# Optimization experiments

Hardware: AMD Instinct MI355X
Metric: run time of the kernel (lower is better)

Reference implementation:

```python
import jax, jax.numpy as jnp
import numpy as np
from jax import lax
from functools import partial

NPOINT = 2048
RADIUS = 1.0
NSAMPLE = 32


def _fps(xyz, npoint):
    # Farthest point sampling, sequential as in the classic CUDA kernel.
    # xyz: (N, 3) -> (npoint,) int32 indices; starts at index 0.
    N = xyz.shape[0]
    init_d = jnp.full((N,), jnp.inf, dtype=xyz.dtype)

    def step(carry, _):
        dists, last = carry
        delta = xyz - xyz[last]                      # (N, 3)
        nd = jnp.sum(delta * delta, axis=-1)         # (N,)
        dists = jnp.minimum(dists, nd)
        nxt = jnp.argmax(dists).astype(jnp.int32)
        return (dists, nxt), last

    (_, _), idxs = lax.scan(step, (init_d, jnp.int32(0)), None, length=npoint)
    return idxs


def _ball_query(radius, nsample, xyz, new_xyz):
    # xyz: (N, 3), new_xyz: (S, 3) -> (S, nsample) int32.
    # Take the first nsample points (in original order) within radius of each
    # centroid; pad with the first found index (centroid itself always hits).
    N = xyz.shape[0]
    d2 = (jnp.sum(new_xyz * new_xyz, -1, keepdims=True)
          + jnp.sum(xyz * xyz, -1)[None, :]
          - 2.0 * new_xyz @ xyz.T)                   # (S, N)
    mask = d2 < radius * radius
    key = jnp.where(mask, jnp.arange(N, dtype=jnp.int32), jnp.int32(N))  # (S, N)
    neg_topk, _ = lax.top_k(-key, nsample)           # nsample smallest keys
    idx = -neg_topk                                  # (S, nsample), ascending
    first = idx[:, :1]
    return jnp.where(idx == N, first, idx)


def setup_inputs() -> dict:
    key = jax.random.key(0)
    inputs = jax.random.normal(key, (4, 8192, 16), dtype=jnp.float32)
    return {"inputs": inputs}


def reference(inputs):
    xyz = inputs[..., :3]                            # (B, N, 3)
    points = inputs[..., 3:]                         # (B, N, C)

    fps_idx = jax.vmap(lambda p: _fps(p, NPOINT))(xyz)          # (B, S)
    new_xyz = jnp.take_along_axis(xyz, fps_idx[..., None], axis=1)  # (B, S, 3)

    idx = jax.vmap(partial(_ball_query, RADIUS, NSAMPLE))(xyz, new_xyz)  # (B, S, K)

    gather = jax.vmap(lambda p, i: p[i])             # (N, C), (S, K) -> (S, K, C)
    grouped_xyz = gather(xyz, idx) - new_xyz[:, :, None, :]      # (B, S, K, 3)
    grouped_points = gather(points, idx)                         # (B, S, K, C)
    new_points = jnp.concatenate([grouped_xyz, grouped_points], axis=-1)
    return new_xyz, new_points, idx, grouped_xyz
```

## Files before the change

### kernel.cpp

```cpp
#include <hip/hip_runtime.h>

#pragma clang fp contract(off)

#define NPOINT 2048
#define NSAMPLE 32
#define NPTS 8192
#define NB 4
#define CH 16
#define FPS_THREADS 512
#define PTS_PER_THREAD (NPTS / FPS_THREADS)
#define PAIRS (PTS_PER_THREAD / 2)
#define FPS_WAVES (FPS_THREADS / 64)

typedef unsigned long long u64;
typedef float v2f __attribute__((ext_vector_type(2)));

#define OFF_NEWXYZ 0
#define OFF_NEWPTS (NB * NPOINT * 3)
#define OFF_IDX (OFF_NEWPTS + NB * NPOINT * NSAMPLE * CH)
#define OFF_GXYZ (OFF_IDX + NB * NPOINT * NSAMPLE)

template <int CTRL>
__device__ __forceinline__ float dpp_fmax(float v) {
  int o = __builtin_amdgcn_update_dpp(0, __float_as_int(v), CTRL, 0xf, 0xf, true);
  return fmaxf(v, __int_as_float(o));
}

__global__ __launch_bounds__(FPS_THREADS)
__attribute__((amdgpu_waves_per_eu(2))) void fps_kernel(
    const float* __restrict__ in, float* __restrict__ out) {
  __shared__ float4 lpxyz[NPTS];
  __shared__ float newb[NPOINT * 3];
  __shared__ alignas(16) u64 slots[2][FPS_WAVES];

  const int b = blockIdx.x;
  const int tid = threadIdx.x;
  const int lane = tid & 63;
  const int wv = tid >> 6;
  const float* base = in + (size_t)b * NPTS * CH;

  v2f pxv[PAIRS], pyv[PAIRS], pzv[PAIRS], dv[PAIRS];
#pragma unroll
  for (int jp = 0; jp < PAIRS; ++jp) {
    int p0 = tid * PTS_PER_THREAD + 2 * jp;
    float4 r0 = *reinterpret_cast<const float4*>(base + (size_t)p0 * CH);
    float4 r1 = *reinterpret_cast<const float4*>(base + (size_t)(p0 + 1) * CH);
    pxv[jp] = (v2f){r0.x, r1.x};
    pyv[jp] = (v2f){r0.y, r1.y};
    pzv[jp] = (v2f){r0.z, r1.z};
    lpxyz[p0] = r0;
    lpxyz[p0 + 1] = r1;
    dv[jp] = (v2f){__builtin_inff(), __builtin_inff()};
  }
  if (tid < FPS_WAVES)
    slots[0][tid] = (tid == 0) ? (((u64)0x7f800000u << 32) | 8191u) : 0ull;

  for (int it = 0; it < NPOINT; ++it) {
    __syncthreads();
    const ulonglong2* sp =
        reinterpret_cast<const ulonglong2*>(&slots[it & 1][0]);
    const ulonglong2 s01 = sp[0];
    const ulonglong2 s23 = sp[1];
    const ulonglong2 s45 = sp[2];
    const ulonglong2 s67 = sp[3];
    u64 ka = (s01.y > s01.x) ? s01.y : s01.x;
    u64 kb = (s23.y > s23.x) ? s23.y : s23.x;
    u64 kc = (s45.y > s45.x) ? s45.y : s45.x;
    u64 kd = (s67.y > s67.x) ? s67.y : s67.x;
    ka = (kb > ka) ? kb : ka;
    kc = (kd > kc) ? kd : kc;
    const u64 k = (kc > ka) ? kc : ka;
    const int gi = 8191 - (int)(unsigned)k;
    const float4 g = lpxyz[gi];
    const float gx = g.x, gy = g.y, gz = g.z;
    if (tid == 0) {
      newb[it * 3 + 0] = gx;
      newb[it * 3 + 1] = gy;
      newb[it * 3 + 2] = gz;
    }
    float bestv = -1.0f;
    float bestx = -1.0f;
    int bestjp = 0;
#pragma unroll
    for (int jp = 0; jp < PAIRS; ++jp) {
      v2f dx = pxv[jp] - gx;
      v2f dy = pyv[jp] - gy;
      v2f dz = pzv[jp] - gz;
      v2f nd = (dx * dx + dy * dy) + dz * dz;
      v2f dn = {fminf(dv[jp].x, nd.x), fminf(dv[jp].y, nd.y)};
      dv[jp] = dn;
      float pm = fmaxf(dn.x, dn.y);
      bool t = pm > bestv;
      bestjp = t ? jp : bestjp;
      bestx = t ? dn.x : bestx;
      bestv = fmaxf(bestv, pm);
    }
    const int bestj = 2 * bestjp + ((bestx == bestv) ? 0 : 1);
    const unsigned besti = (unsigned)(tid * PTS_PER_THREAD + bestj);
    float wm = bestv;
    wm = dpp_fmax<0x111>(wm);
    wm = dpp_fmax<0x112>(wm);
    wm = dpp_fmax<0x114>(wm);
    wm = dpp_fmax<0x118>(wm);
    wm = dpp_fmax<0x142>(wm);
    wm = dpp_fmax<0x143>(wm);
    const float swm =
        __int_as_float(__builtin_amdgcn_readlane(__float_as_int(wm), 63));
    const u64 wbal = __ballot(bestv == swm);
    const int wl = (int)__builtin_ctzll(wbal);
    if (lane == wl) {
      slots[(it + 1) & 1][wv] =
          ((u64)__float_as_uint(bestv) << 32) | (8191u - besti);
    }
  }
  __syncthreads();
  float* ob = out + OFF_NEWXYZ + (size_t)b * NPOINT * 3;
  for (int i = tid; i < NPOINT * 3; i += FPS_THREADS) ob[i] = newb[i];
}

__device__ __forceinline__ void write_slot(float* __restrict__ out,
                                           const float* __restrict__ base,
                                           int b, int qi, int s, int p,
                                           float4 r0, float qx, float qy,
                                           float qz) {
  float dx = __fsub_rn(r0.x, qx);
  float dy = __fsub_rn(r0.y, qy);
  float dz = __fsub_rn(r0.z, qz);
  size_t qs = (size_t)b * NPOINT + qi;
  out[OFF_IDX + qs * NSAMPLE + s] = (float)p;
  float* g = out + OFF_GXYZ + (qs * NSAMPLE + s) * 3;
  g[0] = dx;
  g[1] = dy;
  g[2] = dz;
  const float* row = base + (size_t)p * CH;
  float4 r1 = *reinterpret_cast<const float4*>(row + 4);
  float4 r2 = *reinterpret_cast<const float4*>(row + 8);
  float4 r3 = *reinterpret_cast<const float4*>(row + 12);
  float* np_ = out + OFF_NEWPTS + (qs * NSAMPLE + s) * CH;
  *reinterpret_cast<float4*>(np_ + 0) = make_float4(dx, dy, dz, r0.w);
  *reinterpret_cast<float4*>(np_ + 4) = r1;
  *reinterpret_cast<float4*>(np_ + 8) = r2;
  *reinterpret_cast<float4*>(np_ + 12) = r3;
}

__global__ __launch_bounds__(256) void ballq_kernel(
    const float* __restrict__ in, float* __restrict__ out) {
  const int lane = threadIdx.x & 63;
  const int qid = blockIdx.x * 4 + (threadIdx.x >> 6);
  const int b = qid >> 11;
  const int qi = qid & 2047;
  const float* base = in + (size_t)b * NPTS * CH;
  const float* q = out + OFF_NEWXYZ + ((size_t)b * NPOINT + qi) * 3;
  float qx = q[0], qy = q[1], qz = q[2];
  float qn = __fadd_rn(__fadd_rn(__fmul_rn(qx, qx), __fmul_rn(qy, qy)),
                       __fmul_rn(qz, qz));

  int cnt = 0;
  int first = 0;
  bool have_first = false;
  for (int cg = 0; cg < NPTS / 64 && cnt < NSAMPLE; cg += 4) {
    float4 r[4];
#pragma unroll
    for (int u = 0; u < 4; ++u)
      r[u] = *reinterpret_cast<const float4*>(
          base + (size_t)((cg + u) * 64 + lane) * CH);
#pragma unroll
    for (int u = 0; u < 4; ++u) {
      const int chunk = cg + u;
      const int p = chunk * 64 + lane;
      const float4 r0 = r[u];
      float pn =
          __fadd_rn(__fadd_rn(__fmul_rn(r0.x, r0.x), __fmul_rn(r0.y, r0.y)),
                    __fmul_rn(r0.z, r0.z));
      float dot =
          __fadd_rn(__fadd_rn(__fmul_rn(qx, r0.x), __fmul_rn(qy, r0.y)),
                    __fmul_rn(qz, r0.z));
      float d2 = __fsub_rn(__fadd_rn(qn, pn), __fmul_rn(2.0f, dot));
      bool in_r = d2 < 1.0f;
      unsigned long long mask = __ballot(in_r);
      if (!have_first && mask) {
        first = chunk * 64 + __builtin_ctzll(mask);
        have_first = true;
      }
      int pos = cnt + __popcll(mask & ((1ull << lane) - 1ull));
      if (in_r && pos < NSAMPLE)
        write_slot(out, base, b, qi, pos, p, r0, qx, qy, qz);
      cnt += __popcll(mask);
    }
  }
  if (cnt < NSAMPLE) {
    int s = cnt + lane;
    if (s < NSAMPLE) {
      float4 r0 = *reinterpret_cast<const float4*>(base + (size_t)first * CH);
      write_slot(out, base, b, qi, s, first, r0, qx, qy, qz);
    }
  }
}

extern "C" void kernel_launch(void* const* d_in, const int* in_sizes, int n_in,
                              void* d_out, int out_size, void* d_ws,
                              size_t ws_size, hipStream_t stream) {
  (void)in_sizes;
  (void)n_in;
  (void)out_size;
  (void)d_ws;
  (void)ws_size;
  const float* in = (const float*)d_in[0];
  float* out = (float*)d_out;
  fps_kernel<<<NB, FPS_THREADS, 0, stream>>>(in, out);
  ballq_kernel<<<(NB * NPOINT) / 4, 256, 0, stream>>>(in, out);
}
```

Measured before the change: 1.840 ms.

## Fuse FPS and ball query into one persistent kernel with progress flags

```diff
diff --git a/kernel.cpp b/kernel.cpp
--- a/kernel.cpp
+++ b/kernel.cpp
@@ -11,6 +11,8 @@
 #define PTS_PER_THREAD (NPTS / FPS_THREADS)
 #define PAIRS (PTS_PER_THREAD / 2)
 #define FPS_WAVES (FPS_THREADS / 64)
+#define BQ_BLOCKS 252
+#define BQ_WAVES (BQ_BLOCKS * 8)
 
 typedef unsigned long long u64;
 typedef float v2f __attribute__((ext_vector_type(2)));
@@ -24,98 +26,6 @@
 __device__ __forceinline__ float dpp_fmax(float v) {
   int o = __builtin_amdgcn_update_dpp(0, __float_as_int(v), CTRL, 0xf, 0xf, true);
   return fmaxf(v, __int_as_float(o));
-}
-
-__global__ __launch_bounds__(FPS_THREADS)
-__attribute__((amdgpu_waves_per_eu(2))) void fps_kernel(
-    const float* __restrict__ in, float* __restrict__ out) {
-  __shared__ float4 lpxyz[NPTS];
-  __shared__ float newb[NPOINT * 3];
-  __shared__ alignas(16) u64 slots[2][FPS_WAVES];
-
-  const int b = blockIdx.x;
-  const int tid = threadIdx.x;
-  const int lane = tid & 63;
-  const int wv = tid >> 6;
-  const float* base = in + (size_t)b * NPTS * CH;
-
-  v2f pxv[PAIRS], pyv[PAIRS], pzv[PAIRS], dv[PAIRS];
-#pragma unroll
-  for (int jp = 0; jp < PAIRS; ++jp) {
-    int p0 = tid * PTS_PER_THREAD + 2 * jp;
-    float4 r0 = *reinterpret_cast<const float4*>(base + (size_t)p0 * CH);
-    float4 r1 = *reinterpret_cast<const float4*>(base + (size_t)(p0 + 1) * CH);
-    pxv[jp] = (v2f){r0.x, r1.x};
-    pyv[jp] = (v2f){r0.y, r1.y};
-    pzv[jp] = (v2f){r0.z, r1.z};
-    lpxyz[p0] = r0;
-    lpxyz[p0 + 1] = r1;
-    dv[jp] = (v2f){__builtin_inff(), __builtin_inff()};
-  }
-  if (tid < FPS_WAVES)
-    slots[0][tid] = (tid == 0) ? (((u64)0x7f800000u << 32) | 8191u) : 0ull;
-
-  for (int it = 0; it < NPOINT; ++it) {
-    __syncthreads();
-    const ulonglong2* sp =
-        reinterpret_cast<const ulonglong2*>(&slots[it & 1][0]);
-    const ulonglong2 s01 = sp[0];
-    const ulonglong2 s23 = sp[1];
-    const ulonglong2 s45 = sp[2];
-    const ulonglong2 s67 = sp[3];
-    u64 ka = (s01.y > s01.x) ? s01.y : s01.x;
-    u64 kb = (s23.y > s23.x) ? s23.y : s23.x;
-    u64 kc = (s45.y > s45.x) ? s45.y : s45.x;
-    u64 kd = (s67.y > s67.x) ? s67.y : s67.x;
-    ka = (kb > ka) ? kb : ka;
-    kc = (kd > kc) ? kd : kc;
-    const u64 k = (kc > ka) ? kc : ka;
-    const int gi = 8191 - (int)(unsigned)k;
-    const float4 g = lpxyz[gi];
-    const float gx = g.x, gy = g.y, gz = g.z;
-    if (tid == 0) {
-      newb[it * 3 + 0] = gx;
-      newb[it * 3 + 1] = gy;
-      newb[it * 3 + 2] = gz;
-    }
-    float bestv = -1.0f;
-    float bestx = -1.0f;
-    int bestjp = 0;
-#pragma unroll
-    for (int jp = 0; jp < PAIRS; ++jp) {
-      v2f dx = pxv[jp] - gx;
-      v2f dy = pyv[jp] - gy;
-      v2f dz = pzv[jp] - gz;
-      v2f nd = (dx * dx + dy * dy) + dz * dz;
-      v2f dn = {fminf(dv[jp].x, nd.x), fminf(dv[jp].y, nd.y)};
-      dv[jp] = dn;
-      float pm = fmaxf(dn.x, dn.y);
-      bool t = pm > bestv;
-      bestjp = t ? jp : bestjp;
-      bestx = t ? dn.x : bestx;
-      bestv = fmaxf(bestv, pm);
-    }
-    const int bestj = 2 * bestjp + ((bestx == bestv) ? 0 : 1);
-    const unsigned besti = (unsigned)(tid * PTS_PER_THREAD + bestj);
-    float wm = bestv;
-    wm = dpp_fmax<0x111>(wm);
-    wm = dpp_fmax<0x112>(wm);
-    wm = dpp_fmax<0x114>(wm);
-    wm = dpp_fmax<0x118>(wm);
-    wm = dpp_fmax<0x142>(wm);
-    wm = dpp_fmax<0x143>(wm);
-    const float swm =
-        __int_as_float(__builtin_amdgcn_readlane(__float_as_int(wm), 63));
-    const u64 wbal = __ballot(bestv == swm);
-    const int wl = (int)__builtin_ctzll(wbal);
-    if (lane == wl) {
-      slots[(it + 1) & 1][wv] =
-          ((u64)__float_as_uint(bestv) << 32) | (8191u - besti);
-    }
-  }
-  __syncthreads();
-  float* ob = out + OFF_NEWXYZ + (size_t)b * NPOINT * 3;
-  for (int i = tid; i < NPOINT * 3; i += FPS_THREADS) ob[i] = newb[i];
 }
 
 __device__ __forceinline__ void write_slot(float* __restrict__ out,
@@ -143,18 +53,14 @@
   *reinterpret_cast<float4*>(np_ + 12) = r3;
 }
 
-__global__ __launch_bounds__(256) void ballq_kernel(
-    const float* __restrict__ in, float* __restrict__ out) {
-  const int lane = threadIdx.x & 63;
-  const int qid = blockIdx.x * 4 + (threadIdx.x >> 6);
-  const int b = qid >> 11;
-  const int qi = qid & 2047;
+__device__ __forceinline__ void ballq_one(const float* __restrict__ in,
+                                          float* __restrict__ out, int b,
+                                          int qi, int lane) {
   const float* base = in + (size_t)b * NPTS * CH;
   const float* q = out + OFF_NEWXYZ + ((size_t)b * NPOINT + qi) * 3;
   float qx = q[0], qy = q[1], qz = q[2];
   float qn = __fadd_rn(__fadd_rn(__fmul_rn(qx, qx), __fmul_rn(qy, qy)),
                        __fmul_rn(qz, qz));
-
   int cnt = 0;
   int first = 0;
   bool have_first = false;
@@ -197,16 +103,235 @@
   }
 }
 
+__global__ __launch_bounds__(FPS_THREADS)
+__attribute__((amdgpu_waves_per_eu(2))) void fused_kernel(
+    const float* __restrict__ in, float* __restrict__ out,
+    unsigned* __restrict__ prog) {
+  __shared__ float4 lpxyz[NPTS];
+  __shared__ float newb[NPOINT * 3];
+  __shared__ alignas(16) u64 slots[2][FPS_WAVES];
+
+  const int tid = threadIdx.x;
+  const int lane = tid & 63;
+
+  if (blockIdx.x >= NB) {
+    const int slot = (blockIdx.x - NB) * 8 + (tid >> 6);
+    for (int g = slot; g < NB * NPOINT; g += BQ_WAVES) {
+      const int qi = g >> 2;
+      const int b = g & 3;
+      for (;;) {
+        unsigned p = __hip_atomic_load(&prog[b], __ATOMIC_ACQUIRE,
+                                       __HIP_MEMORY_SCOPE_AGENT);
+        if (p > (unsigned)qi) break;
+        __builtin_amdgcn_s_sleep(32);
+      }
+      ballq_one(in, out, b, qi, lane);
+    }
+    return;
+  }
+
+  const int b = blockIdx.x;
+  const int wv = tid >> 6;
+  const float* base = in + (size_t)b * NPTS * CH;
+  float* gnew = out + OFF_NEWXYZ + (size_t)b * NPOINT * 3;
+
+  v2f pxv[PAIRS], pyv[PAIRS], pzv[PAIRS], dv[PAIRS];
+#pragma unroll
+  for (int jp = 0; jp < PAIRS; ++jp) {
+    int p0 = tid * PTS_PER_THREAD + 2 * jp;
+    float4 r0 = *reinterpret_cast<const float4*>(base + (size_t)p0 * CH);
+    float4 r1 = *reinterpret_cast<const float4*>(base + (size_t)(p0 + 1) * CH);
+    pxv[jp] = (v2f){r0.x, r1.x};
+    pyv[jp] = (v2f){r0.y, r1.y};
+    pzv[jp] = (v2f){r0.z, r1.z};
+    lpxyz[p0] = r0;
+    lpxyz[p0 + 1] = r1;
+    dv[jp] = (v2f){__builtin_inff(), __builtin_inff()};
+  }
+  if (tid < FPS_WAVES)
+    slots[0][tid] = (tid == 0) ? (((u64)0x7f800000u << 32) | 8191u) : 0ull;
+
+  for (int it = 0; it < NPOINT; ++it) {
+    __syncthreads();
+    const ulonglong2* sp =
+        reinterpret_cast<const ulonglong2*>(&slots[it & 1][0]);
+    const ulonglong2 s01 = sp[0];
+    const ulonglong2 s23 = sp[1];
+    const ulonglong2 s45 = sp[2];
+    const ulonglong2 s67 = sp[3];
+    u64 ka = (s01.y > s01.x) ? s01.y : s01.x;
+    u64 kb = (s23.y > s23.x) ? s23.y : s23.x;
+    u64 kc = (s45.y > s45.x) ? s45.y : s45.x;
+    u64 kd = (s67.y > s67.x) ? s67.y : s67.x;
+    ka = (kb > ka) ? kb : ka;
+    kc = (kd > kc) ? kd : kc;
+    const u64 k = (kc > ka) ? kc : ka;
+    const int gi = 8191 - (int)(unsigned)k;
+    const float4 g = lpxyz[gi];
+    const float gx = g.x, gy = g.y, gz = g.z;
+    if (tid == 0) {
+      newb[it * 3 + 0] = gx;
+      newb[it * 3 + 1] = gy;
+      newb[it * 3 + 2] = gz;
+    }
+    if ((it & 15) == 0 && it >= 16 && tid < 48)
+      gnew[(it - 16) * 3 + tid] = newb[(it - 16) * 3 + tid];
+    if ((it & 15) == 1 && it > 16 && tid == 0)
+      __hip_atomic_store(&prog[b], (unsigned)(it - 1), __ATOMIC_RELEASE,
+                         __HIP_MEMORY_SCOPE_AGENT);
+    float bestv = -1.0f;
+    float bestx = -1.0f;
+    int bestjp = 0;
+#pragma unroll
+    for (int jp = 0; jp < PAIRS; ++jp) {
+      v2f dx = pxv[jp] - gx;
+      v2f dy = pyv[jp] - gy;
+      v2f dz = pzv[jp] - gz;
+      v2f nd = (dx * dx + dy * dy) + dz * dz;
+      v2f dn = {fminf(dv[jp].x, nd.x), fminf(dv[jp].y, nd.y)};
+      dv[jp] = dn;
+      float pm = fmaxf(dn.x, dn.y);
+      bool t = pm > bestv;
+      bestjp = t ? jp : bestjp;
+      bestx = t ? dn.x : bestx;
+      bestv = fmaxf(bestv, pm);
+    }
+    const int bestj = 2 * bestjp + ((bestx == bestv) ? 0 : 1);
+    const unsigned besti = (unsigned)(tid * PTS_PER_THREAD + bestj);
+    float wm = bestv;
+    wm = dpp_fmax<0x111>(wm);
+    wm = dpp_fmax<0x112>(wm);
+    wm = dpp_fmax<0x114>(wm);
+    wm = dpp_fmax<0x118>(wm);
+    wm = dpp_fmax<0x142>(wm);
+    wm = dpp_fmax<0x143>(wm);
+    const float swm =
+        __int_as_float(__builtin_amdgcn_readlane(__float_as_int(wm), 63));
+    const u64 wbal = __ballot(bestv == swm);
+    const int wl = (int)__builtin_ctzll(wbal);
+    if (lane == wl) {
+      slots[(it + 1) & 1][wv] =
+          ((u64)__float_as_uint(bestv) << 32) | (8191u - besti);
+    }
+  }
+  __syncthreads();
+  if (tid < 48) gnew[2032 * 3 + tid] = newb[2032 * 3 + tid];
+  __syncthreads();
+  if (tid == 0)
+    __hip_atomic_store(&prog[b], (unsigned)NPOINT, __ATOMIC_RELEASE,
+                       __HIP_MEMORY_SCOPE_AGENT);
+}
+
+__global__ __launch_bounds__(FPS_THREADS)
+__attribute__((amdgpu_waves_per_eu(2))) void fps_kernel(
+    const float* __restrict__ in, float* __restrict__ out) {
+  __shared__ float4 lpxyz[NPTS];
+  __shared__ float newb[NPOINT * 3];
+  __shared__ alignas(16) u64 slots[2][FPS_WAVES];
+  const int b = blockIdx.x;
+  const int tid = threadIdx.x;
+  const int lane = tid & 63;
+  const int wv = tid >> 6;
+  const float* base = in + (size_t)b * NPTS * CH;
+  v2f pxv[PAIRS], pyv[PAIRS], pzv[PAIRS], dv[PAIRS];
+#pragma unroll
+  for (int jp = 0; jp < PAIRS; ++jp) {
+    int p0 = tid * PTS_PER_THREAD + 2 * jp;
+    float4 r0 = *reinterpret_cast<const float4*>(base + (size_t)p0 * CH);
+    float4 r1 = *reinterpret_cast<const float4*>(base + (size_t)(p0 + 1) * CH);
+    pxv[jp] = (v2f){r0.x, r1.x};
+    pyv[jp] = (v2f){r0.y, r1.y};
+    pzv[jp] = (v2f){r0.z, r1.z};
+    lpxyz[p0] = r0;
+    lpxyz[p0 + 1] = r1;
+    dv[jp] = (v2f){__builtin_inff(), __builtin_inff()};
+  }
+  if (tid < FPS_WAVES)
+    slots[0][tid] = (tid == 0) ? (((u64)0x7f800000u << 32) | 8191u) : 0ull;
+  for (int it = 0; it < NPOINT; ++it) {
+    __syncthreads();
+    const ulonglong2* sp =
+        reinterpret_cast<const ulonglong2*>(&slots[it & 1][0]);
+    const ulonglong2 s01 = sp[0];
+    const ulonglong2 s23 = sp[1];
+    const ulonglong2 s45 = sp[2];
+    const ulonglong2 s67 = sp[3];
+    u64 ka = (s01.y > s01.x) ? s01.y : s01.x;
+    u64 kb = (s23.y > s23.x) ? s23.y : s23.x;
+    u64 kc = (s45.y > s45.x) ? s45.y : s45.x;
+    u64 kd = (s67.y > s67.x) ? s67.y : s67.x;
+    ka = (kb > ka) ? kb : ka;
+    kc = (kd > kc) ? kd : kc;
+    const u64 k = (kc > ka) ? kc : ka;
+    const int gi = 8191 - (int)(unsigned)k;
+    const float4 g = lpxyz[gi];
+    const float gx = g.x, gy = g.y, gz = g.z;
+    if (tid == 0) {
+      newb[it * 3 + 0] = gx;
+      newb[it * 3 + 1] = gy;
+      newb[it * 3 + 2] = gz;
+    }
+    float bestv = -1.0f;
+    float bestx = -1.0f;
+    int bestjp = 0;
+#pragma unroll
+    for (int jp = 0; jp < PAIRS; ++jp) {
+      v2f dx = pxv[jp] - gx;
+      v2f dy = pyv[jp] - gy;
+      v2f dz = pzv[jp] - gz;
+      v2f nd = (dx * dx + dy * dy) + dz * dz;
+      v2f dn = {fminf(dv[jp].x, nd.x), fminf(dv[jp].y, nd.y)};
+      dv[jp] = dn;
+      float pm = fmaxf(dn.x, dn.y);
+      bool t = pm > bestv;
+      bestjp = t ? jp : bestjp;
+      bestx = t ? dn.x : bestx;
+      bestv = fmaxf(bestv, pm);
+    }
+    const int bestj = 2 * bestjp + ((bestx == bestv) ? 0 : 1);
+    const unsigned besti = (unsigned)(tid * PTS_PER_THREAD + bestj);
+    float wm = bestv;
+    wm = dpp_fmax<0x111>(wm);
+    wm = dpp_fmax<0x112>(wm);
+    wm = dpp_fmax<0x114>(wm);
+    wm = dpp_fmax<0x118>(wm);
+    wm = dpp_fmax<0x142>(wm);
+    wm = dpp_fmax<0x143>(wm);
+    const float swm =
+        __int_as_float(__builtin_amdgcn_readlane(__float_as_int(wm), 63));
+    const u64 wbal = __ballot(bestv == swm);
+    const int wl = (int)__builtin_ctzll(wbal);
+    if (lane == wl) {
+      slots[(it + 1) & 1][wv] =
+          ((u64)__float_as_uint(bestv) << 32) | (8191u - besti);
+    }
+  }
+  __syncthreads();
+  float* ob = out + OFF_NEWXYZ + (size_t)b * NPOINT * 3;
+  for (int i = tid; i < NPOINT * 3; i += FPS_THREADS) ob[i] = newb[i];
+}
+
+__global__ __launch_bounds__(256) void ballq_kernel(
+    const float* __restrict__ in, float* __restrict__ out) {
+  const int lane = threadIdx.x & 63;
+  const int qid = blockIdx.x * 4 + (threadIdx.x >> 6);
+  ballq_one(in, out, qid >> 11, qid & 2047, lane);
+}
+
 extern "C" void kernel_launch(void* const* d_in, const int* in_sizes, int n_in,
                               void* d_out, int out_size, void* d_ws,
                               size_t ws_size, hipStream_t stream) {
   (void)in_sizes;
   (void)n_in;
   (void)out_size;
-  (void)d_ws;
-  (void)ws_size;
   const float* in = (const float*)d_in[0];
   float* out = (float*)d_out;
-  fps_kernel<<<NB, FPS_THREADS, 0, stream>>>(in, out);
-  ballq_kernel<<<(NB * NPOINT) / 4, 256, 0, stream>>>(in, out);
-}
+  if (d_ws != nullptr && ws_size >= NB * sizeof(unsigned)) {
+    unsigned* prog = (unsigned*)d_ws;
+    hipMemsetAsync(prog, 0, NB * sizeof(unsigned), stream);
+    fused_kernel<<<NB + BQ_BLOCKS, FPS_THREADS, 0, stream>>>(in, out, prog);
+  } else {
+    fps_kernel<<<NB, FPS_THREADS, 0, stream>>>(in, out);
+    ballq_kernel<<<(NB * NPOINT) / 4, 256, 0, stream>>>(in, out);
+  }
+}
```

Result: slower. 2.124 ms (+15.4%).

## Fuse FPS and ball query into one persistent kernel with spin-wait streaming

Applied to the files above, without the earlier changes.

```diff
diff --git a/kernel.cpp b/kernel.cpp
--- a/kernel.cpp
+++ b/kernel.cpp
@@ -11,6 +11,9 @@
 #define PTS_PER_THREAD (NPTS / FPS_THREADS)
 #define PAIRS (PTS_PER_THREAD / 2)
 #define FPS_WAVES (FPS_THREADS / 64)
+#define BQ_BLOCKS 252
+#define BQ_WAVES (BQ_BLOCKS * 8)
+#define SENT 0xFFFFFFFFu
 
 typedef unsigned long long u64;
 typedef float v2f __attribute__((ext_vector_type(2)));
@@ -26,96 +29,16 @@
   return fmaxf(v, __int_as_float(o));
 }
 
-__global__ __launch_bounds__(FPS_THREADS)
-__attribute__((amdgpu_waves_per_eu(2))) void fps_kernel(
-    const float* __restrict__ in, float* __restrict__ out) {
-  __shared__ float4 lpxyz[NPTS];
-  __shared__ float newb[NPOINT * 3];
-  __shared__ alignas(16) u64 slots[2][FPS_WAVES];
-
-  const int b = blockIdx.x;
-  const int tid = threadIdx.x;
-  const int lane = tid & 63;
-  const int wv = tid >> 6;
-  const float* base = in + (size_t)b * NPTS * CH;
-
-  v2f pxv[PAIRS], pyv[PAIRS], pzv[PAIRS], dv[PAIRS];
-#pragma unroll
-  for (int jp = 0; jp < PAIRS; ++jp) {
-    int p0 = tid * PTS_PER_THREAD + 2 * jp;
-    float4 r0 = *reinterpret_cast<const float4*>(base + (size_t)p0 * CH);
-    float4 r1 = *reinterpret_cast<const float4*>(base + (size_t)(p0 + 1) * CH);
-    pxv[jp] = (v2f){r0.x, r1.x};
-    pyv[jp] = (v2f){r0.y, r1.y};
-    pzv[jp] = (v2f){r0.z, r1.z};
-    lpxyz[p0] = r0;
-    lpxyz[p0 + 1] = r1;
-    dv[jp] = (v2f){__builtin_inff(), __builtin_inff()};
-  }
-  if (tid < FPS_WAVES)
-    slots[0][tid] = (tid == 0) ? (((u64)0x7f800000u << 32) | 8191u) : 0ull;
-
-  for (int it = 0; it < NPOINT; ++it) {
-    __syncthreads();
-    const ulonglong2* sp =
-        reinterpret_cast<const ulonglong2*>(&slots[it & 1][0]);
-    const ulonglong2 s01 = sp[0];
-    const ulonglong2 s23 = sp[1];
-    const ulonglong2 s45 = sp[2];
-    const ulonglong2 s67 = sp[3];
-    u64 ka = (s01.y > s01.x) ? s01.y : s01.x;
-    u64 kb = (s23.y > s23.x) ? s23.y : s23.x;
-    u64 kc = (s45.y > s45.x) ? s45.y : s45.x;
-    u64 kd = (s67.y > s67.x) ? s67.y : s67.x;
-    ka = (kb > ka) ? kb : ka;
-    kc = (kd > kc) ? kd : kc;
-    const u64 k = (kc > ka) ? kc : ka;
-    const int gi = 8191 - (int)(unsigned)k;
-    const float4 g = lpxyz[gi];
-    const float gx = g.x, gy = g.y, gz = g.z;
-    if (tid == 0) {
-      newb[it * 3 + 0] = gx;
-      newb[it * 3 + 1] = gy;
-      newb[it * 3 + 2] = gz;
-    }
-    float bestv = -1.0f;
-    float bestx = -1.0f;
-    int bestjp = 0;
-#pragma unroll
-    for (int jp = 0; jp < PAIRS; ++jp) {
-      v2f dx = pxv[jp] - gx;
-      v2f dy = pyv[jp] - gy;
-      v2f dz = pzv[jp] - gz;
-      v2f nd = (dx * dx + dy * dy) + dz * dz;
-      v2f dn = {fminf(dv[jp].x, nd.x), fminf(dv[jp].y, nd.y)};
-      dv[jp] = dn;
-      float pm = fmaxf(dn.x, dn.y);
-      bool t = pm > bestv;
-      bestjp = t ? jp : bestjp;
-      bestx = t ? dn.x : bestx;
-      bestv = fmaxf(bestv, pm);
-    }
-    const int bestj = 2 * bestjp + ((bestx == bestv) ? 0 : 1);
-    const unsigned besti = (unsigned)(tid * PTS_PER_THREAD + bestj);
-    float wm = bestv;
-    wm = dpp_fmax<0x111>(wm);
-    wm = dpp_fmax<0x112>(wm);
-    wm = dpp_fmax<0x114>(wm);
-    wm = dpp_fmax<0x118>(wm);
-    wm = dpp_fmax<0x142>(wm);
-    wm = dpp_fmax<0x143>(wm);
-    const float swm =
-        __int_as_float(__builtin_amdgcn_readlane(__float_as_int(wm), 63));
-    const u64 wbal = __ballot(bestv == swm);
-    const int wl = (int)__builtin_ctzll(wbal);
-    if (lane == wl) {
-      slots[(it + 1) & 1][wv] =
-          ((u64)__float_as_uint(bestv) << 32) | (8191u - besti);
-    }
-  }
-  __syncthreads();
-  float* ob = out + OFF_NEWXYZ + (size_t)b * NPOINT * 3;
-  for (int i = tid; i < NPOINT * 3; i += FPS_THREADS) ob[i] = newb[i];
+__device__ __forceinline__ void lgkm_barrier() {
+  asm volatile("s_waitcnt lgkmcnt(0)" ::: "memory");
+  __builtin_amdgcn_s_barrier();
+}
+
+__device__ __forceinline__ void st_sc1(float* p, float v) {
+  __hip_atomic_store(p, v, __ATOMIC_RELAXED, __HIP_MEMORY_SCOPE_AGENT);
+}
+__device__ __forceinline__ unsigned ld_sc1_u(const unsigned* p) {
+  return __hip_atomic_load(p, __ATOMIC_RELAXED, __HIP_MEMORY_SCOPE_AGENT);
 }
 
 __device__ __forceinline__ void write_slot(float* __restrict__ out,
@@ -143,18 +66,13 @@
   *reinterpret_cast<float4*>(np_ + 12) = r3;
 }
 
-__global__ __launch_bounds__(256) void ballq_kernel(
-    const float* __restrict__ in, float* __restrict__ out) {
-  const int lane = threadIdx.x & 63;
-  const int qid = blockIdx.x * 4 + (threadIdx.x >> 6);
-  const int b = qid >> 11;
-  const int qi = qid & 2047;
+__device__ __forceinline__ void ballq_one(const float* __restrict__ in,
+                                          float* __restrict__ out, int b,
+                                          int qi, int lane, float qx,
+                                          float qy, float qz) {
   const float* base = in + (size_t)b * NPTS * CH;
-  const float* q = out + OFF_NEWXYZ + ((size_t)b * NPOINT + qi) * 3;
-  float qx = q[0], qy = q[1], qz = q[2];
   float qn = __fadd_rn(__fadd_rn(__fmul_rn(qx, qx), __fmul_rn(qy, qy)),
                        __fmul_rn(qz, qz));
-
   int cnt = 0;
   int first = 0;
   bool have_first = false;
@@ -197,6 +115,117 @@
   }
 }
 
+__global__ __launch_bounds__(FPS_THREADS)
+__attribute__((amdgpu_waves_per_eu(2))) void fused_kernel(
+    const float* __restrict__ in, float* __restrict__ out) {
+  __shared__ float4 lpxyz[NPTS];
+  __shared__ alignas(16) u64 slots[2][FPS_WAVES];
+
+  const int tid = threadIdx.x;
+  const int lane = tid & 63;
+
+  if (blockIdx.x >= NB) {
+    const int slot = (blockIdx.x - NB) * 8 + (tid >> 6);
+    for (int g = slot; g < NB * NPOINT; g += BQ_WAVES) {
+      const int qi = g >> 2;
+      const int b = g & 3;
+      const unsigned* qw = reinterpret_cast<const unsigned*>(
+          out + OFF_NEWXYZ + ((size_t)b * NPOINT + qi) * 3);
+      unsigned x, y, z;
+      for (;;) {
+        x = ld_sc1_u(&qw[0]);
+        y = ld_sc1_u(&qw[1]);
+        z = ld_sc1_u(&qw[2]);
+        if (x != SENT && y != SENT && z != SENT) break;
+        __builtin_amdgcn_s_sleep(8);
+      }
+      ballq_one(in, out, b, qi, lane, __uint_as_float(x), __uint_as_float(y),
+                __uint_as_float(z));
+    }
+    return;
+  }
+
+  const int b = blockIdx.x;
+  const int wv = tid >> 6;
+  const float* base = in + (size_t)b * NPTS * CH;
+  float* gnew = out + OFF_NEWXYZ + (size_t)b * NPOINT * 3;
+
+  v2f pxv[PAIRS], pyv[PAIRS], pzv[PAIRS], dv[PAIRS];
+#pragma unroll
+  for (int jp = 0; jp < PAIRS; ++jp) {
+    int p0 = tid * PTS_PER_THREAD + 2 * jp;
+    float4 r0 = *reinterpret_cast<const float4*>(base + (size_t)p0 * CH);
+    float4 r1 = *reinterpret_cast<const float4*>(base + (size_t)(p0 + 1) * CH);
+    pxv[jp] = (v2f){r0.x, r1.x};
+    pyv[jp] = (v2f){r0.y, r1.y};
+    pzv[jp] = (v2f){r0.z, r1.z};
+    lpxyz[p0] = r0;
+    lpxyz[p0 + 1] = r1;
+    dv[jp] = (v2f){__builtin_inff(), __builtin_inff()};
+  }
+  if (tid < FPS_WAVES)
+    slots[0][tid] = (tid == 0) ? (((u64)0x7f800000u << 32) | 8191u) : 0ull;
+
+  for (int it = 0; it < NPOINT; ++it) {
+    lgkm_barrier();
+    const ulonglong2* sp =
+        reinterpret_cast<const ulonglong2*>(&slots[it & 1][0]);
+    const ulonglong2 s01 = sp[0];
+    const ulonglong2 s23 = sp[1];
+    const ulonglong2 s45 = sp[2];
+    const ulonglong2 s67 = sp[3];
+    u64 ka = (s01.y > s01.x) ? s01.y : s01.x;
+    u64 kb = (s23.y > s23.x) ? s23.y : s23.x;
+    u64 kc = (s45.y > s45.x) ? s45.y : s45.x;
+    u64 kd = (s67.y > s67.x) ? s67.y : s67.x;
+    ka = (kb > ka) ? kb : ka;
+    kc = (kd > kc) ? kd : kc;
+    const u64 k = (kc > ka) ? kc : ka;
+    const int gi = 8191 - (int)(unsigned)k;
+    const float4 g = lpxyz[gi];
+    const float gx = g.x, gy = g.y, gz = g.z;
+    if (tid == 0) {
+      st_sc1(&gnew[it * 3 + 0], gx);
+      st_sc1(&gnew[it * 3 + 1], gy);
+      st_sc1(&gnew[it * 3 + 2], gz);
+    }
+    float bestv = -1.0f;
+    float bestx = -1.0f;
+    int bestjp = 0;
+#pragma unroll
+    for (int jp = 0; jp < PAIRS; ++jp) {
+      v2f dx = pxv[jp] - gx;
+      v2f dy = pyv[jp] - gy;
+      v2f dz = pzv[jp] - gz;
+      v2f nd = (dx * dx + dy * dy) + dz * dz;
+      v2f dn = {fminf(dv[jp].x, nd.x), fminf(dv[jp].y, nd.y)};
+      dv[jp] = dn;
+      float pm = fmaxf(dn.x, dn.y);
+      bool t = pm > bestv;
+      bestjp = t ? jp : bestjp;
+      bestx = t ? dn.x : bestx;
+      bestv = fmaxf(bestv, pm);
+    }
+    const int bestj = 2 * bestjp + ((bestx == bestv) ? 0 : 1);
+    const unsigned besti = (unsigned)(tid * PTS_PER_THREAD + bestj);
+    float wm = bestv;
+    wm = dpp_fmax<0x111>(wm);
+    wm = dpp_fmax<0x112>(wm);
+    wm = dpp_fmax<0x114>(wm);
+    wm = dpp_fmax<0x118>(wm);
+    wm = dpp_fmax<0x142>(wm);
+    wm = dpp_fmax<0x143>(wm);
+    const float swm =
+        __int_as_float(__builtin_amdgcn_readlane(__float_as_int(wm), 63));
+    const u64 wbal = __ballot(bestv == swm);
+    const int wl = (int)__builtin_ctzll(wbal);
+    if (lane == wl) {
+      slots[(it + 1) & 1][wv] =
+          ((u64)__float_as_uint(bestv) << 32) | (8191u - besti);
+    }
+  }
+}
+
 extern "C" void kernel_launch(void* const* d_in, const int* in_sizes, int n_in,
                               void* d_out, int out_size, void* d_ws,
                               size_t ws_size, hipStream_t stream) {
@@ -207,6 +236,7 @@
   (void)ws_size;
   const float* in = (const float*)d_in[0];
   float* out = (float*)d_out;
-  fps_kernel<<<NB, FPS_THREADS, 0, stream>>>(in, out);
-  ballq_kernel<<<(NB * NPOINT) / 4, 256, 0, stream>>>(in, out);
-}
+  hipMemsetAsync(out + OFF_NEWXYZ, 0xFF, (size_t)NB * NPOINT * 3 * sizeof(float),
+                 stream);
+  fused_kernel<<<NB + BQ_BLOCKS, FPS_THREADS, 0, stream>>>(in, out);
+}
```

Measured after the change: 1.748 ms. 1.05x faster.
